# Performance work log

Hardware: AMD Instinct MI355X
Metric: run time of the kernel (lower is better)

Reference implementation:

```python
import jax, jax.numpy as jnp
import numpy as np

B, N, C, H, BS = 4, 4096, 1024, 16, 64
E = C // H          # head dim = 64
EPS = 1e-3

def setup_inputs() -> dict:
    key = jax.random.key(0)
    k0, k1, k2, k3 = jax.random.split(key, 4)
    x = jax.random.normal(k0, (B, N, C), jnp.float32)
    qkv_w = jax.random.normal(k1, (3 * C, C), jnp.float32) * 0.02
    proj_w = jax.random.normal(k2, (C, C), jnp.float32) * 0.02
    proj_b = jax.random.normal(k3, (C,), jnp.float32) * 0.02
    return {"x": x, "qkv_w": qkv_w, "proj_w": proj_w, "proj_b": proj_b}

def reference(x, qkv_w, proj_w, proj_b):
    b, n, c = x.shape
    h, e, bs = H, E, BS
    u = n // bs  # number of buckets
    # qkv projection (no bias), split to (B,H,N,e) per q/k/v
    qkv = (x @ qkv_w.T).reshape(b, n, 3, h, e).transpose(2, 0, 3, 1, 4)
    q, k, v = qkv[0], qkv[1], qkv[2]
    # feature maps: softmax(q) scaled, exp(k)
    q = jax.nn.softmax(q, axis=-1) * (e ** -0.5)
    k = jnp.exp(k)
    # bucket along sequence: (B,H,U,BS,e)
    b_q = q.reshape(b, h, u, bs, e)
    b_k = k.reshape(b, h, u, bs, e)
    b_v = v.reshape(b, h, u, bs, e)
    # per-bucket k sums and inter-bucket cumulative sums
    b_k_cumsum = jnp.cumsum(b_k.sum(axis=-2), axis=-2)            # (B,H,U,e)
    context = jnp.einsum('bhund,bhune->bhude', b_k, b_v)          # (B,H,U,e,e)
    context = jnp.cumsum(context, axis=2)
    # exclusive shift by one bucket (bucket_size > 1 path in original)
    context = jnp.concatenate(
        [jnp.zeros_like(context[:, :, :1]), context[:, :, :-1]], axis=2)
    b_k_cumsum = jnp.concatenate(
        [jnp.zeros_like(b_k_cumsum[:, :, :1]), b_k_cumsum[:, :, :-1]], axis=2)
    # normalizer, clamped from below at eps
    D_inv = 1.0 / jnp.maximum(
        jnp.einsum('bhud,bhund->bhun', b_k_cumsum, b_q), EPS)
    attn = jnp.einsum('bhund,bhude,bhun->bhune', b_q, context, D_inv)
    out = attn.reshape(b, h, n, e).transpose(0, 2, 1, 3).reshape(b, n, c)
    # output projection (dropouts are identity at eval)
    return out @ proj_w.T + proj_b
```

## Files before the change

### kernel.cpp

```cpp
#include <hip/hip_runtime.h>
#include <stdint.h>


typedef unsigned short u16;
typedef unsigned int u32;
typedef u16   u16x4  __attribute__((ext_vector_type(4)));
typedef u16   u16x8  __attribute__((ext_vector_type(8)));
typedef float f32x4  __attribute__((ext_vector_type(4)));
typedef float float4v __attribute__((ext_vector_type(4)));
typedef __bf16 bf16x8 __attribute__((ext_vector_type(8)));

__device__ __forceinline__ u16 f2bf(float f) {
  return __builtin_bit_cast(u16, (__bf16)f);
}
__device__ __forceinline__ float bf2f(u16 h) {
  return (float)__builtin_bit_cast(__bf16, h);
}

__device__ __forceinline__ void stage16(const u16* g, u16* l) {
  __builtin_amdgcn_global_load_lds(
      (const __attribute__((address_space(1))) u32*)g,
      (__attribute__((address_space(3))) u32*)l, 16, 0, 0);
}

__global__ __launch_bounds__(256) void cvt_all(
    const float* __restrict__ x, const float* __restrict__ wqf,
    const float* __restrict__ wpf, u16* __restrict__ xb,
    u16* __restrict__ wq, u16* __restrict__ wp) {
  int i = blockIdx.x * 256 + threadIdx.x;
  const float* in; u16* out; int j;
  if (i < 4194304)      { in = x;   out = xb; j = i; }
  else if (i < 4980736) { in = wqf; out = wq; j = i - 4194304; }
  else                  { in = wpf; out = wp; j = i - 4980736; }
  float4v v = reinterpret_cast<const float4v*>(in)[j];
  u16x4 o;
  o.x = f2bf(v.x); o.y = f2bf(v.y); o.z = f2bf(v.z); o.w = f2bf(v.w);
  reinterpret_cast<u16x4*>(out)[j] = o;
}

template <int EPI>
__global__ __launch_bounds__(512, 2) void gemm256(
    const u16* __restrict__ A,
    const u16* __restrict__ B,
    const float* __restrict__ bias,
    float* __restrict__ Cf,
    u16* __restrict__ Qf, u16* __restrict__ Kt, u16* __restrict__ Vt,
    float* __restrict__ ksum,
    int N, int K, int NT) {
  __shared__ u16 As[2][2][256][32];
  __shared__ u16 Bs[2][2][256][32];
  const int tid = threadIdx.x, lane = tid & 63, wave = tid >> 6;
  const int wm = wave >> 2, wn = wave & 3;
  const int l15 = lane & 15, l4 = lane >> 4;
  const int ntn = N >> 8;
  const int cpx = gridDim.x >> 3;
  const int bid = (blockIdx.x & 7) * cpx + (blockIdx.x >> 3);
  const int bm = bid / ntn, bn = bid % ntn;

  const int srow = tid >> 2;
  const int gsl8 = ((tid & 3) ^ ((tid >> 3) & 3)) * 8;
  const u16* Ag = A + (size_t)(bm * 256 + srow) * K + gsl8;
  const u16* Bg = B + (size_t)(bn * 256 + srow) * K + gsl8;
  const size_t rj = (size_t)128 * K;
  const int slotr = (l4 ^ ((l15 >> 1) & 3)) * 8;

  f32x4 acc[8][4] = {};
  bf16x8 a0, a1, a2, a3, a4, a5, a6, a7, b0, b1, b2, b3;

#define STG(P, buf, kh, kt)                                        \
  { const u16* g_ = P##g + (kt) + (kh) * 32;                       \
    stage16(g_,      &P##s[buf][kh][wave * 16][0]);                \
    stage16(g_ + rj, &P##s[buf][kh][128 + wave * 16][0]); }

#define LDA(r0_, r1_, r2_, r3_, kk, mh)                                  \
  { const u16* p_ = &As[cur][kk][wm * 128 + (mh) * 64 + l15][0] + slotr; \
    r0_ = *(const bf16x8*)(p_);                                          \
    r1_ = *(const bf16x8*)(p_ + 512);                                    \
    r2_ = *(const bf16x8*)(p_ + 1024);                                   \
    r3_ = *(const bf16x8*)(p_ + 1536); }

#define LDB(kk)                                                    \
  { const u16* p_ = &Bs[cur][kk][wn * 64 + l15][0] + slotr;        \
    b0 = *(const bf16x8*)(p_);                                     \
    b1 = *(const bf16x8*)(p_ + 512);                               \
    b2 = *(const bf16x8*)(p_ + 1024);                              \
    b3 = *(const bf16x8*)(p_ + 1536); }

#define MM(x, y, z) z = __builtin_amdgcn_mfma_f32_16x16x32_bf16(x, y, z, 0, 0, 0)
#define MFMA16(mb, x0, x1, x2, x3)                                 \
  __builtin_amdgcn_s_setprio(1);                                   \
  MM(x0, b0, acc[(mb) + 0][0]); MM(x0, b1, acc[(mb) + 0][1]);      \
  MM(x0, b2, acc[(mb) + 0][2]); MM(x0, b3, acc[(mb) + 0][3]);      \
  MM(x1, b0, acc[(mb) + 1][0]); MM(x1, b1, acc[(mb) + 1][1]);      \
  MM(x1, b2, acc[(mb) + 1][2]); MM(x1, b3, acc[(mb) + 1][3]);      \
  MM(x2, b0, acc[(mb) + 2][0]); MM(x2, b1, acc[(mb) + 2][1]);      \
  MM(x2, b2, acc[(mb) + 2][2]); MM(x2, b3, acc[(mb) + 2][3]);      \
  MM(x3, b0, acc[(mb) + 3][0]); MM(x3, b1, acc[(mb) + 3][1]);      \
  MM(x3, b2, acc[(mb) + 3][2]); MM(x3, b3, acc[(mb) + 3][3]);      \
  __builtin_amdgcn_s_setprio(0);

#define BARF()                                                     \
  { asm volatile("" ::: "memory");                                 \
    __builtin_amdgcn_s_barrier();                                  \
    asm volatile("" ::: "memory"); }

  STG(A, 0, 0, 0) STG(B, 0, 0, 0) STG(A, 0, 1, 0) STG(B, 0, 1, 0)
  asm volatile("s_waitcnt vmcnt(0)" ::: "memory");
  __builtin_amdgcn_s_barrier();
  asm volatile("" ::: "memory");

  for (int t = 0; t < NT; ++t) {
    const int cur = t & 1, nxt = cur ^ 1;
    const int ktn = (t + 1) << 6;
    const bool pre = (t + 1 < NT);
    LDB(0)
    LDA(a0, a1, a2, a3, 0, 0)
    LDA(a4, a5, a6, a7, 0, 1)
    if (pre) STG(A, nxt, 0, ktn)
    MFMA16(0, a0, a1, a2, a3)
    if (pre) STG(B, nxt, 0, ktn)
    MFMA16(4, a4, a5, a6, a7)
    if (pre) { asm volatile("s_waitcnt vmcnt(4)" ::: "memory"); }
    else     { asm volatile("s_waitcnt vmcnt(0)" ::: "memory"); }
    BARF()
    LDB(1)
    LDA(a0, a1, a2, a3, 1, 0)
    LDA(a4, a5, a6, a7, 1, 1)
    if (pre) STG(A, nxt, 1, ktn)
    MFMA16(0, a0, a1, a2, a3)
    if (pre) STG(B, nxt, 1, ktn)
    MFMA16(4, a4, a5, a6, a7)
    if (pre) { asm volatile("s_waitcnt vmcnt(4)" ::: "memory"); }
    BARF()
  }
#undef STG
#undef LDA
#undef LDB
#undef MM
#undef MFMA16
#undef BARF

  const int row0 = bm * 256 + wm * 128 + l4 * 4;
  const int col0 = bn * 256 + wn * 64 + l15;
  if constexpr (EPI == 0) {
    float bv[4];
#pragma unroll
    for (int ni = 0; ni < 4; ++ni) bv[ni] = bias[col0 + ni * 16];
#pragma unroll
    for (int mi = 0; mi < 8; ++mi)
#pragma unroll
      for (int i = 0; i < 4; ++i) {
        size_t r = (size_t)(row0 + mi * 16 + i) * N;
#pragma unroll
        for (int ni = 0; ni < 4; ++ni)
          Cf[r + col0 + ni * 16] = acc[mi][ni][i] + bv[ni];
      }
  } else {
    const int i3 = bn >> 2;
    const int h  = ((bn & 3) << 2) + wn;
    if (i3 == 0) {
#pragma unroll
      for (int mi = 0; mi < 8; ++mi)
#pragma unroll
        for (int i = 0; i < 4; ++i) {
          const int row = row0 + mi * 16 + i;
          const int bb = row >> 12, uu = (row >> 6) & 63, nn = row & 63;
          u16* op = Qf + ((size_t)((bb * 16 + h) * 64 + uu)) * 4096
                        + nn * 64 + l15;
          float v0 = acc[mi][0][i], v1 = acc[mi][1][i];
          float v2 = acc[mi][2][i], v3 = acc[mi][3][i];
          float mx = fmaxf(fmaxf(v0, v1), fmaxf(v2, v3));
          mx = fmaxf(mx, __shfl_xor(mx, 1));
          mx = fmaxf(mx, __shfl_xor(mx, 2));
          mx = fmaxf(mx, __shfl_xor(mx, 4));
          mx = fmaxf(mx, __shfl_xor(mx, 8));
          float e0 = __expf(v0 - mx), e1 = __expf(v1 - mx);
          float e2 = __expf(v2 - mx), e3 = __expf(v3 - mx);
          float s = e0 + e1 + e2 + e3;
          s += __shfl_xor(s, 1); s += __shfl_xor(s, 2);
          s += __shfl_xor(s, 4); s += __shfl_xor(s, 8);
          float inv = 0.125f / s;
          op[0]  = f2bf(e0 * inv); op[16] = f2bf(e1 * inv);
          op[32] = f2bf(e2 * inv); op[48] = f2bf(e3 * inv);
        }
    } else if (i3 == 1) {
      float sk0[4] = {0.f, 0.f, 0.f, 0.f};
      float sk1[4] = {0.f, 0.f, 0.f, 0.f};
#pragma unroll
      for (int mi = 0; mi < 8; ++mi) {
        const int row = row0 + mi * 16;
        const int bb = row >> 12, uu = (row >> 6) & 63, nn = row & 63;
        u16* op = Kt + ((size_t)((bb * 16 + h) * 64 + uu)) * 4096 + nn;
#pragma unroll
        for (int ni = 0; ni < 4; ++ni) {
          float e0 = __expf(acc[mi][ni][0]);
          float e1 = __expf(acc[mi][ni][1]);
          float e2 = __expf(acc[mi][ni][2]);
          float e3 = __expf(acc[mi][ni][3]);
          u16x4 o;
          o.x = f2bf(e0); o.y = f2bf(e1); o.z = f2bf(e2); o.w = f2bf(e3);
          *reinterpret_cast<u16x4*>(op + (ni * 16 + l15) * 64) = o;
          if (mi < 4) sk0[ni] += e0 + e1 + e2 + e3;
          else        sk1[ni] += e0 + e1 + e2 + e3;
        }
      }
#pragma unroll
      for (int ni = 0; ni < 4; ++ni) {
        sk0[ni] += __shfl_xor(sk0[ni], 16); sk0[ni] += __shfl_xor(sk0[ni], 32);
        sk1[ni] += __shfl_xor(sk1[ni], 16); sk1[ni] += __shfl_xor(sk1[ni], 32);
      }
      if (lane < 16) {
        const int nb0 = bm * 256 + wm * 128;
        const size_t bkt0 = (size_t)(((nb0 >> 12) * 16 + h) * 64 + ((nb0 >> 6) & 63));
#pragma unroll
        for (int ni = 0; ni < 4; ++ni) {
          ksum[bkt0 * 64 + ni * 16 + l15]       = sk0[ni];
          ksum[(bkt0 + 1) * 64 + ni * 16 + l15] = sk1[ni];
        }
      }
    } else {
#pragma unroll
      for (int mi = 0; mi < 8; ++mi) {
        const int row = row0 + mi * 16;
        const int bb = row >> 12, uu = (row >> 6) & 63, nn = row & 63;
        u16* op = Vt + ((size_t)((bb * 16 + h) * 64 + uu)) * 4096 + nn;
#pragma unroll
        for (int ni = 0; ni < 4; ++ni) {
          u16x4 o;
          o.x = f2bf(acc[mi][ni][0]); o.y = f2bf(acc[mi][ni][1]);
          o.z = f2bf(acc[mi][ni][2]); o.w = f2bf(acc[mi][ni][3]);
          *reinterpret_cast<u16x4*>(op + (ni * 16 + l15) * 64) = o;
        }
      }
    }
  }
}

__global__ __launch_bounds__(256) void scanctx2(
    const u16* __restrict__ Kt,
    const u16* __restrict__ Vt,
    u16* __restrict__ ctxb) {
  const int bh = blockIdx.x >> 2, ec = blockIdx.x & 3;
  const int tid = threadIdx.x, lane = tid & 63, wave = tid >> 6;
  const int l15 = lane & 15, l4 = lane >> 4;
  __shared__ u16 KtL[2][64][72];
  __shared__ u16 VtL[2][16][72];

  const size_t bbase = (size_t)bh * 64 * 4096;
  const int kr0 = tid >> 3, ks0 = (tid & 7) * 8;
  const int kr1 = 32 + kr0;
  const bool dov = tid < 128;
  const int vr = tid >> 3, vs = (tid & 7) * 8;

  f32x4 acc = {0.f, 0.f, 0.f, 0.f};

  u16x8 k0 = *reinterpret_cast<const u16x8*>(Kt + bbase + kr0 * 64 + ks0);
  u16x8 k1 = *reinterpret_cast<const u16x8*>(Kt + bbase + kr1 * 64 + ks0);
  u16x8 v0 = {};
  if (dov) v0 = *reinterpret_cast<const u16x8*>(Vt + bbase + (ec * 16 + vr) * 64 + vs);
  *reinterpret_cast<u16x8*>(&KtL[0][kr0][ks0]) = k0;
  *reinterpret_cast<u16x8*>(&KtL[0][kr1][ks0]) = k1;
  if (dov) *reinterpret_cast<u16x8*>(&VtL[0][vr][vs]) = v0;
  __syncthreads();

  for (int u = 0; u < 64; ++u) {
    const int cur = u & 1, nxt = cur ^ 1;
    const bool pre = (u + 1 < 64);
    if (pre) {
      const size_t nb = bbase + (size_t)(u + 1) * 4096;
      k0 = *reinterpret_cast<const u16x8*>(Kt + nb + kr0 * 64 + ks0);
      k1 = *reinterpret_cast<const u16x8*>(Kt + nb + kr1 * 64 + ks0);
      if (dov) v0 = *reinterpret_cast<const u16x8*>(Vt + nb + (ec * 16 + vr) * 64 + vs);
    }
    {
      u16* cb = ctxb + (bbase + (size_t)u * 4096) + wave * 16 + l15;
#pragma unroll
      for (int i = 0; i < 4; ++i)
        cb[(ec * 16 + l4 * 4 + i) * 64] = f2bf(acc[i]);
    }
#pragma unroll
    for (int kk = 0; kk < 2; ++kk) {
      bf16x8 av = *reinterpret_cast<const bf16x8*>(&VtL[cur][l15][kk * 32 + l4 * 8]);
      bf16x8 bk = *reinterpret_cast<const bf16x8*>(&KtL[cur][wave * 16 + l15][kk * 32 + l4 * 8]);
      acc = __builtin_amdgcn_mfma_f32_16x16x32_bf16(av, bk, acc, 0, 0, 0);
    }
    if (pre) {
      *reinterpret_cast<u16x8*>(&KtL[nxt][kr0][ks0]) = k0;
      *reinterpret_cast<u16x8*>(&KtL[nxt][kr1][ks0]) = k1;
      if (dov) *reinterpret_cast<u16x8*>(&VtL[nxt][vr][vs]) = v0;
    }
    __syncthreads();
  }
}

__global__ __launch_bounds__(64) void scanK(float* __restrict__ ksum) {
  const int bh = blockIdx.x;
  float* p = ksum + (size_t)bh * 4096 + threadIdx.x;
  float run = 0.f;
#define LK(i) p[(size_t)(i) * 64]
  float c0 = LK(0), c1 = LK(1), c2 = LK(2), c3 = LK(3);
  for (int u = 0; u < 64; u += 4) {
    const int i4 = u + 4 < 64 ? u + 4 : 63, i5 = u + 5 < 64 ? u + 5 : 63;
    const int i6 = u + 6 < 64 ? u + 6 : 63, i7 = u + 7 < 64 ? u + 7 : 63;
    float n0 = LK(i4), n1 = LK(i5), n2 = LK(i6), n3 = LK(i7);
    LK(u) = run;     run += c0;
    LK(u + 1) = run; run += c1;
    LK(u + 2) = run; run += c2;
    LK(u + 3) = run; run += c3;
    c0 = n0; c1 = n1; c2 = n2; c3 = n3;
  }
#undef LK
}

__global__ __launch_bounds__(256) void apply(
    const u16* __restrict__ Q, const u16* __restrict__ ctxc,
    const float* __restrict__ kcum, u16* __restrict__ AT) {
  const int bid = blockIdx.x;
  const int u = bid & 63, bh = bid >> 6, b = bh >> 4, h = bh & 15;
  const int tid = threadIdx.x, lane = tid & 63, wave = tid >> 6;
  const int l15 = lane & 15, l4 = lane >> 4;
  __shared__ float kc[64];
  __shared__ float dp[64][4];
  __shared__ float dinv[64];

  const size_t base = (size_t)bid * 4096;
  const u16* Qu = Q + base;
  if (tid < 64) kc[tid] = kcum[(size_t)bid * 64 + tid];
  __syncthreads();
  {
    int n = tid & 63, q = tid >> 6;
    const u16* qp = Qu + n * 64 + q * 16;
    float a = 0.f;
#pragma unroll
    for (int j = 0; j < 16; ++j) a += bf2f(qp[j]) * kc[q * 16 + j];
    dp[n][q] = a;
  }
  __syncthreads();
  if (tid < 64)
    dinv[tid] = 1.f / fmaxf(dp[tid][0] + dp[tid][1] + dp[tid][2] + dp[tid][3], 1e-3f);
  __syncthreads();

  f32x4 acc[4] = {};
  const u16* Cu = ctxc + base;
#pragma unroll
  for (int kk = 0; kk < 2; ++kk) {
    bf16x8 aq = *reinterpret_cast<const bf16x8*>(Qu + (wave * 16 + l15) * 64 + kk * 32 + l4 * 8);
#pragma unroll
    for (int ni = 0; ni < 4; ++ni) {
      bf16x8 bc = *reinterpret_cast<const bf16x8*>(Cu + (ni * 16 + l15) * 64 + kk * 32 + l4 * 8);
      acc[ni] = __builtin_amdgcn_mfma_f32_16x16x32_bf16(aq, bc, acc[ni], 0, 0, 0);
    }
  }
  const size_t orow = ((size_t)b * 4096 + u * 64 + wave * 16 + l4 * 4) * 1024 + h * 64;
#pragma unroll
  for (int i = 0; i < 4; ++i) {
    float di = dinv[wave * 16 + l4 * 4 + i];
#pragma unroll
    for (int ni = 0; ni < 4; ++ni)
      AT[orow + (size_t)i * 1024 + ni * 16 + l15] = f2bf(acc[ni][i] * di);
  }
}

extern "C" void kernel_launch(void* const* d_in, const int* in_sizes, int n_in,
                              void* d_out, int out_size, void* d_ws, size_t ws_size,
                              hipStream_t stream) {
  (void)in_sizes; (void)n_in; (void)out_size; (void)ws_size;
  const float* x      = (const float*)d_in[0];
  const float* qkv_w  = (const float*)d_in[1];
  const float* proj_w = (const float*)d_in[2];
  const float* proj_b = (const float*)d_in[3];
  float* out = (float*)d_out;

  char* ws = (char*)d_ws;
  u16* xb    = (u16*)(ws);
  u16* wq    = (u16*)(ws + 33554432);
  u16* wp    = (u16*)(ws + 39845888);
  u16* Qf    = (u16*)(ws + 41943040);
  u16* Kt    = (u16*)(ws + 75497472);
  u16* Vt    = (u16*)(ws + 109051904);
  u16* ctxb  = (u16*)(ws + 142606336);
  float* ksum = (float*)(ws + 176160768);
  u16* AT    = Kt;

  cvt_all<<<dim3(20480), dim3(256), 0, stream>>>(x, qkv_w, proj_w, xb, wq, wp);

  gemm256<2><<<dim3(64 * 12), dim3(512), 0, stream>>>(
      xb, wq, nullptr, nullptr, Qf, Kt, Vt, ksum, 3072, 1024, 16);
  scanK<<<dim3(64), dim3(64), 0, stream>>>(ksum);
  scanctx2<<<dim3(256), dim3(256), 0, stream>>>(Kt, Vt, ctxb);
  apply<<<dim3(4096), dim3(256), 0, stream>>>(Qf, ctxb, ksum, AT);
  gemm256<0><<<dim3(64 * 4), dim3(512), 0, stream>>>(
      AT, wp, proj_b, out, nullptr, nullptr, nullptr, nullptr, 1024, 1024, 16);
}
```

Before: 240.6 us.

## Process two buckets per barrier in scanctx2 and compute normalizer in registers in apply

The context scan kernel now loads and stages two buckets per iteration, so there is one __syncthreads per pair of buckets instead of one per bucket. LDS use doubles in exchange. The apply kernel drops its scalar dot-product pass through shared memory and two barriers. Instead it computes the q·kcum normalizer from the already-loaded MFMA Q fragments and combines it across lanes with shuffles. This removes redundant Q global reads and synchronization in apply.

After: 234.3 us. -2.6%, faster.

```diff
diff --git a/kernel.cpp b/kernel.cpp
--- a/kernel.cpp
+++ b/kernel.cpp
@@ -243,54 +243,59 @@
   const int bh = blockIdx.x >> 2, ec = blockIdx.x & 3;
   const int tid = threadIdx.x, lane = tid & 63, wave = tid >> 6;
   const int l15 = lane & 15, l4 = lane >> 4;
-  __shared__ u16 KtL[2][64][72];
-  __shared__ u16 VtL[2][16][72];
+  __shared__ u16 KtL[2][2][64][72];
+  __shared__ u16 VtL[2][2][16][72];
 
   const size_t bbase = (size_t)bh * 64 * 4096;
-  const int kr0 = tid >> 3, ks0 = (tid & 7) * 8;
+  const int kr0 = tid >> 3, ks = (tid & 7) * 8;
   const int kr1 = 32 + kr0;
   const bool dov = tid < 128;
   const int vr = tid >> 3, vs = (tid & 7) * 8;
 
   f32x4 acc = {0.f, 0.f, 0.f, 0.f};
-
-  u16x8 k0 = *reinterpret_cast<const u16x8*>(Kt + bbase + kr0 * 64 + ks0);
-  u16x8 k1 = *reinterpret_cast<const u16x8*>(Kt + bbase + kr1 * 64 + ks0);
-  u16x8 v0 = {};
-  if (dov) v0 = *reinterpret_cast<const u16x8*>(Vt + bbase + (ec * 16 + vr) * 64 + vs);
-  *reinterpret_cast<u16x8*>(&KtL[0][kr0][ks0]) = k0;
-  *reinterpret_cast<u16x8*>(&KtL[0][kr1][ks0]) = k1;
-  if (dov) *reinterpret_cast<u16x8*>(&VtL[0][vr][vs]) = v0;
+  u16x8 ka0, ka1, kb0, kb1, va = {}, vb = {};
+
+#define GLD(u_, kx0, kx1, vx)                                          \
+  { const size_t nb = bbase + (size_t)(u_) * 4096;                     \
+    kx0 = *reinterpret_cast<const u16x8*>(Kt + nb + kr0 * 64 + ks);    \
+    kx1 = *reinterpret_cast<const u16x8*>(Kt + nb + kr1 * 64 + ks);    \
+    if (dov) vx = *reinterpret_cast<const u16x8*>(                     \
+        Vt + nb + (ec * 16 + vr) * 64 + vs); }
+#define LWR(buf, j, kx0, kx1, vx)                                      \
+  { *reinterpret_cast<u16x8*>(&KtL[buf][j][kr0][ks]) = kx0;            \
+    *reinterpret_cast<u16x8*>(&KtL[buf][j][kr1][ks]) = kx1;            \
+    if (dov) *reinterpret_cast<u16x8*>(&VtL[buf][j][vr][vs]) = vx; }
+#define ACC(buf, j)                                                    \
+  _Pragma("unroll")                                                    \
+  for (int kk = 0; kk < 2; ++kk) {                                     \
+    bf16x8 av = *reinterpret_cast<const bf16x8*>(                      \
+        &VtL[buf][j][l15][kk * 32 + l4 * 8]);                          \
+    bf16x8 bk = *reinterpret_cast<const bf16x8*>(                      \
+        &KtL[buf][j][wave * 16 + l15][kk * 32 + l4 * 8]);              \
+    acc = __builtin_amdgcn_mfma_f32_16x16x32_bf16(av, bk, acc, 0, 0, 0); }
+
+  GLD(0, ka0, ka1, va) GLD(1, kb0, kb1, vb)
+  LWR(0, 0, ka0, ka1, va) LWR(0, 1, kb0, kb1, vb)
   __syncthreads();
 
-  for (int u = 0; u < 64; ++u) {
-    const int cur = u & 1, nxt = cur ^ 1;
-    const bool pre = (u + 1 < 64);
-    if (pre) {
-      const size_t nb = bbase + (size_t)(u + 1) * 4096;
-      k0 = *reinterpret_cast<const u16x8*>(Kt + nb + kr0 * 64 + ks0);
-      k1 = *reinterpret_cast<const u16x8*>(Kt + nb + kr1 * 64 + ks0);
-      if (dov) v0 = *reinterpret_cast<const u16x8*>(Vt + nb + (ec * 16 + vr) * 64 + vs);
-    }
-    {
-      u16* cb = ctxb + (bbase + (size_t)u * 4096) + wave * 16 + l15;
-#pragma unroll
-      for (int i = 0; i < 4; ++i)
-        cb[(ec * 16 + l4 * 4 + i) * 64] = f2bf(acc[i]);
-    }
-#pragma unroll
-    for (int kk = 0; kk < 2; ++kk) {
-      bf16x8 av = *reinterpret_cast<const bf16x8*>(&VtL[cur][l15][kk * 32 + l4 * 8]);
-      bf16x8 bk = *reinterpret_cast<const bf16x8*>(&KtL[cur][wave * 16 + l15][kk * 32 + l4 * 8]);
-      acc = __builtin_amdgcn_mfma_f32_16x16x32_bf16(av, bk, acc, 0, 0, 0);
-    }
-    if (pre) {
-      *reinterpret_cast<u16x8*>(&KtL[nxt][kr0][ks0]) = k0;
-      *reinterpret_cast<u16x8*>(&KtL[nxt][kr1][ks0]) = k1;
-      if (dov) *reinterpret_cast<u16x8*>(&VtL[nxt][vr][vs]) = v0;
-    }
+  for (int u = 0; u < 64; u += 2) {
+    const int cur = (u >> 1) & 1, nxt = cur ^ 1;
+    const bool pre = (u + 2 < 64);
+    if (pre) { GLD(u + 2, ka0, ka1, va) GLD(u + 3, kb0, kb1, vb) }
+    u16* cb0 = ctxb + bbase + (size_t)u * 4096 + wave * 16 + l15;
+#pragma unroll
+    for (int i = 0; i < 4; ++i) cb0[(ec * 16 + l4 * 4 + i) * 64] = f2bf(acc[i]);
+    ACC(cur, 0)
+    u16* cb1 = cb0 + 4096;
+#pragma unroll
+    for (int i = 0; i < 4; ++i) cb1[(ec * 16 + l4 * 4 + i) * 64] = f2bf(acc[i]);
+    ACC(cur, 1)
+    if (pre) { LWR(nxt, 0, ka0, ka1, va) LWR(nxt, 1, kb0, kb1, vb) }
     __syncthreads();
   }
+#undef GLD
+#undef LWR
+#undef ACC
 }
 
 __global__ __launch_bounds__(64) void scanK(float* __restrict__ ksum) {
@@ -320,44 +325,44 @@
   const int tid = threadIdx.x, lane = tid & 63, wave = tid >> 6;
   const int l15 = lane & 15, l4 = lane >> 4;
   __shared__ float kc[64];
-  __shared__ float dp[64][4];
-  __shared__ float dinv[64];
 
   const size_t base = (size_t)bid * 4096;
-  const u16* Qu = Q + base;
   if (tid < 64) kc[tid] = kcum[(size_t)bid * 64 + tid];
   __syncthreads();
-  {
-    int n = tid & 63, q = tid >> 6;
-    const u16* qp = Qu + n * 64 + q * 16;
-    float a = 0.f;
-#pragma unroll
-    for (int j = 0; j < 16; ++j) a += bf2f(qp[j]) * kc[q * 16 + j];
-    dp[n][q] = a;
-  }
-  __syncthreads();
-  if (tid < 64)
-    dinv[tid] = 1.f / fmaxf(dp[tid][0] + dp[tid][1] + dp[tid][2] + dp[tid][3], 1e-3f);
-  __syncthreads();
+
+  bf16x8 aq[2];
+  float dpart = 0.f;
+#pragma unroll
+  for (int kk = 0; kk < 2; ++kk) {
+    aq[kk] = *reinterpret_cast<const bf16x8*>(
+        Q + base + (wave * 16 + l15) * 64 + kk * 32 + l4 * 8);
+    const float* kcp = &kc[kk * 32 + l4 * 8];
+#pragma unroll
+    for (int j = 0; j < 8; ++j) dpart += (float)aq[kk][j] * kcp[j];
+  }
+  dpart += __shfl_xor(dpart, 16);
+  dpart += __shfl_xor(dpart, 32);
+  const float dinv_self = 1.f / fmaxf(dpart, 1e-3f);
+  float dv[4];
+#pragma unroll
+  for (int i = 0; i < 4; ++i) dv[i] = __shfl(dinv_self, l4 * 4 + i);
 
   f32x4 acc[4] = {};
   const u16* Cu = ctxc + base;
 #pragma unroll
-  for (int kk = 0; kk < 2; ++kk) {
-    bf16x8 aq = *reinterpret_cast<const bf16x8*>(Qu + (wave * 16 + l15) * 64 + kk * 32 + l4 * 8);
+  for (int kk = 0; kk < 2; ++kk)
 #pragma unroll
     for (int ni = 0; ni < 4; ++ni) {
-      bf16x8 bc = *reinterpret_cast<const bf16x8*>(Cu + (ni * 16 + l15) * 64 + kk * 32 + l4 * 8);
-      acc[ni] = __builtin_amdgcn_mfma_f32_16x16x32_bf16(aq, bc, acc[ni], 0, 0, 0);
+      bf16x8 bc = *reinterpret_cast<const bf16x8*>(
+          Cu + (ni * 16 + l15) * 64 + kk * 32 + l4 * 8);
+      acc[ni] = __builtin_amdgcn_mfma_f32_16x16x32_bf16(aq[kk], bc, acc[ni], 0, 0, 0);
     }
-  }
   const size_t orow = ((size_t)b * 4096 + u * 64 + wave * 16 + l4 * 4) * 1024 + h * 64;
 #pragma unroll
   for (int i = 0; i < 4; ++i) {
-    float di = dinv[wave * 16 + l4 * 4 + i];
 #pragma unroll
     for (int ni = 0; ni < 4; ++ni)
-      AT[orow + (size_t)i * 1024 + ni * 16 + l15] = f2bf(acc[ni][i] * di);
+      AT[orow + (size_t)i * 1024 + ni * 16 + l15] = f2bf(acc[ni][i] * dv[i]);
   }
 }
 
```
